# Kernel optimization log

Measured on AMD Instinct MI355X. Metric: run time of the kernel, lower is better.

## Reference

```python
import jax, jax.numpy as jnp
import numpy as np

N_GENES = 15135
N_CMT = 1000
HID = 64


def _gcn_norm(edge_index, n):
    # add self-loops, compute symmetric normalization deg^-1/2 * deg^-1/2
    loop = jnp.arange(n, dtype=edge_index.dtype)
    src = jnp.concatenate([edge_index[0], loop])
    dst = jnp.concatenate([edge_index[1], loop])
    deg = jax.ops.segment_sum(jnp.ones_like(src, dtype=jnp.float32), dst, num_segments=n)
    dinv = jnp.where(deg > 0, 1.0 / jnp.sqrt(deg), 0.0)
    return src, dst, dinv[src] * dinv[dst]


def _gcn_conv(x, W, b, src, dst, norm, n):
    h = x @ W                                  # [bs, N, H]
    m = h[:, src, :] * norm[None, :, None]     # gather messages [bs, E, H]
    out = jnp.zeros_like(h).at[:, dst, :].add(m)
    return out + b


def setup_inputs():
    key = jax.random.key(0)
    ks = jax.random.split(key, 16)
    bs, nf, hfc, ncls, E, P = 8, 64, 128, 2, 242160, 120000
    s = 0.05
    return {
        "x": jax.random.normal(ks[0], (bs, N_GENES, nf), jnp.float32),
        "batch": jnp.zeros((bs,), jnp.int32),
        "edge_index": jax.random.randint(ks[1], (2, E), 0, N_GENES),
        "path_row": jax.random.randint(ks[2], (P,), 0, N_GENES),
        "path_col": jax.random.randint(ks[3], (P,), 0, N_CMT),
        "W1": jax.random.normal(ks[4], (nf, HID), jnp.float32) * s,
        "b1": jnp.zeros((HID,), jnp.float32),
        "W2": jax.random.normal(ks[5], (HID, HID), jnp.float32) * s,
        "b2": jnp.zeros((HID,), jnp.float32),
        "W3": jax.random.normal(ks[6], (HID, HID), jnp.float32) * s,
        "b3": jnp.zeros((HID,), jnp.float32),
        "fcW": jax.random.normal(ks[7], (3 * HID, 1), jnp.float32) * s,
        "fcb": jnp.zeros((1,), jnp.float32),
        "l1W": jax.random.normal(ks[8], (N_CMT, hfc), jnp.float32) * s,
        "l1b": jnp.zeros((hfc,), jnp.float32),
        "l2W": jax.random.normal(ks[9], (hfc, ncls), jnp.float32) * s,
        "l2b": jnp.zeros((ncls,), jnp.float32),
    }


def reference(x, batch, edge_index, path_row, path_col,
              W1, b1, W2, b2, W3, b3, fcW, fcb, l1W, l1b, l2W, l2b):
    bs, n = x.shape[0], x.shape[1]
    src, dst, norm = _gcn_norm(edge_index, n)

    x1 = jax.nn.relu(_gcn_conv(x, W1, b1, src, dst, norm, n))
    x2 = jax.nn.relu(_gcn_conv(x1, W2, b2, src, dst, norm, n))
    x3 = jax.nn.relu(_gcn_conv(x2, W3, b3, src, dst, norm, n))
    # mode='cat': torch.stack(xs, -1).view(bs, N, -1) -> layout [..., h*L + l]
    xc = jnp.stack([x1, x2, x3], axis=-1).reshape(bs, n, HID * 3)

    # pathway pooling: scatter_mean(x[row], col) over node axis
    xt = jnp.transpose(xc, (1, 0, 2))            # [N, bs, F]
    g = xt[path_row]                             # [P, bs, F]
    sums = jax.ops.segment_sum(g, path_col, num_segments=N_CMT)
    cnt = jax.ops.segment_sum(jnp.ones_like(path_col, dtype=xc.dtype), path_col, num_segments=N_CMT)
    pooled = sums / jnp.maximum(cnt, 1.0)[:, None, None]   # [n_cmt, bs, F]
    pooled = jnp.transpose(pooled, (1, 0, 2)).reshape(-1, HID * 3)  # [bs*n_cmt, F]

    h = (pooled @ fcW + fcb).reshape(bs, N_CMT)   # fc -> view(-1, n_cmt)
    h = jax.nn.relu(h @ l1W + l1b)                # (dropout is identity in eval)
    h = h @ l2W + l2b
    return jax.nn.log_softmax(h, axis=-1)
```

## Files before the change

### kernel.cpp

```cpp
#include <hip/hip_runtime.h>
#include <hip/hip_bf16.h>
#include <hip/hip_fp16.h>
#include <math.h>

#define HID 64

#if defined(__has_builtin)
#if __has_builtin(__builtin_amdgcn_cvt_pk_f32_fp8) && __has_builtin(__builtin_amdgcn_cvt_pk_fp8_f32)
#define HWFP8 1
#endif
#endif

typedef float vfloat2 __attribute__((ext_vector_type(2)));


__device__ __forceinline__ unsigned short f2bf(float x) {
    unsigned int u = __float_as_uint(x);
    unsigned int r = u + 0x7fffu + ((u >> 16) & 1u);
    return (unsigned short)(r >> 16);
}

#ifndef HWFP8
__device__ __forceinline__ unsigned int enc8_sw(float a) {
    unsigned short hb = __half_as_ushort(__float2half(a));
    unsigned int r = (unsigned int)hb + 0x7fu + ((hb >> 8) & 1u);
    return (r >> 8) & 0xffu;
}
__device__ __forceinline__ float dec8_sw(unsigned int b) {
    return __half2float(__ushort_as_half((unsigned short)(b << 8)));
}
#endif

__device__ __forceinline__ unsigned int enc4(float a, float b, float c, float d) {
#ifdef HWFP8
    int r = __builtin_amdgcn_cvt_pk_fp8_f32(a, b, 0, false);
    r = __builtin_amdgcn_cvt_pk_fp8_f32(c, d, r, true);
    return (unsigned int)r;
#else
    return enc8_sw(a) | (enc8_sw(b) << 8) | (enc8_sw(c) << 16) | (enc8_sw(d) << 24);
#endif
}

__device__ __forceinline__ void dec4(unsigned int w, float* f) {
#ifdef HWFP8
    vfloat2 a = __builtin_amdgcn_cvt_pk_f32_fp8((int)w, false);
    vfloat2 b = __builtin_amdgcn_cvt_pk_f32_fp8((int)w, true);
    f[0] = a.x; f[1] = a.y; f[2] = b.x; f[3] = b.y;
#else
    f[0] = dec8_sw(w & 0xffu); f[1] = dec8_sw((w >> 8) & 0xffu);
    f[2] = dec8_sw((w >> 16) & 0xffu); f[3] = dec8_sw(w >> 24);
#endif
}

__device__ __forceinline__ void dec8(uint2 g, float* f) {
    dec4(g.x, f);
    dec4(g.y, f + 4);
}


__global__ __launch_bounds__(256) void k_pre_count(const int* __restrict__ edst, int* __restrict__ deg, int E,
                                                   const int* __restrict__ pcol, int* __restrict__ ccnt, int P) {
    int gth = blockIdx.x * blockDim.x + threadIdx.x;
    int GT = gridDim.x * blockDim.x;
    for (int e = gth; e < E; e += GT) atomicAdd(&deg[edst[e]], 1);
    for (int p = gth; p < P; p += GT) atomicAdd(&ccnt[pcol[p]], 1);
}

__global__ __launch_bounds__(256) void k_pre_scan(const int* __restrict__ deg, int* __restrict__ rowoff, int N,
                                                  const int* __restrict__ ccnt, int* __restrict__ coff, int NC,
                                                  float* __restrict__ dinv) {
    __shared__ int part[256];
    int t = threadIdx.x;
    int gth = blockIdx.x * blockDim.x + t;
    int GT = gridDim.x * blockDim.x;
    for (int i = gth; i < N; i += GT) dinv[i] = rsqrtf((float)(deg[i] + 1));

    const int* cnt = nullptr; int* off = nullptr; int n = 0;
    if (blockIdx.x == 0)      { cnt = deg;  off = rowoff; n = N; }
    else if (blockIdx.x == 1) { cnt = ccnt; off = coff;   n = NC; }
    else return;

    int CH = (n + 255) >> 8;
    int lo = min(t * CH, n), hi = min(lo + CH, n);
    int sum = 0;
    for (int i = lo; i < hi; ++i) sum += cnt[i];
    part[t] = sum;
    __syncthreads();
    for (int o = 1; o < 256; o <<= 1) {
        int v = (t >= o) ? part[t - o] : 0;
        __syncthreads();
        part[t] += v;
        __syncthreads();
    }
    int run = (t == 0) ? 0 : part[t - 1];
    for (int i = lo; i < hi; ++i) { off[i] = run; run += cnt[i]; }
    if (t == 255) off[n] = run;
}

__global__ __launch_bounds__(256) void k_pre_scatter(const int* __restrict__ esrc, const int* __restrict__ edst,
                                                     const float* __restrict__ dinv, const int* __restrict__ rowoff,
                                                     int* __restrict__ fill, int* __restrict__ ssrc,
                                                     float* __restrict__ snorm, int E,
                                                     const int* __restrict__ prow, const int* __restrict__ pcol,
                                                     const int* __restrict__ coff, int* __restrict__ cfill,
                                                     int* __restrict__ crow, int P) {
    int gth = blockIdx.x * blockDim.x + threadIdx.x;
    int GT = gridDim.x * blockDim.x;
    for (int e = gth; e < E; e += GT) {
        int s = esrc[e], d = edst[e];
        int pos = rowoff[d] + atomicAdd(&fill[d], 1);
        ssrc[pos]  = s;
        snorm[pos] = dinv[s] * dinv[d];
    }
    for (int p = gth; p < P; p += GT) {
        int c = pcol[p];
        int pos = coff[c] + atomicAdd(&cfill[c], 1);
        crow[pos] = prow[p];
    }
}


template<int MODE>
__global__ __launch_bounds__(256) void k_gemm_rt(const void* __restrict__ Xv,
                                                 const float* __restrict__ W,
                                                 unsigned int* __restrict__ Yq,
                                                 float S, int N, int rowsTot) {
    __shared__ float sW[64 * 64];
    __shared__ float sXT[64 * 68];
    int t = threadIdx.x;
    int r0 = blockIdx.x * 64;

#pragma unroll
    for (int i = 0; i < 16; ++i) sW[t + i * 256] = W[t + i * 256];

    {
        int row = t & 63;
        int kg = t >> 6;
        int gr = r0 + row;
        bool ok = gr < rowsTot;
        const float* Xf = (const float*)Xv;
        const unsigned short* Xh = (const unsigned short*)Xv;
#pragma unroll
        for (int i = 0; i < 4; ++i) {
            int k = (kg + i * 4) * 4;
            float4 v = make_float4(0.f, 0.f, 0.f, 0.f);
            if (ok) {
                if (MODE == 0) {
                    int n = gr >> 3, b = gr & 7;
                    v = *(const float4*)&Xf[((size_t)b * N + n) * 64 + k];
                } else {
                    ushort4 u = *(const ushort4*)&Xh[(size_t)gr * 64 + k];
                    v.x = __uint_as_float(((unsigned int)u.x) << 16);
                    v.y = __uint_as_float(((unsigned int)u.y) << 16);
                    v.z = __uint_as_float(((unsigned int)u.z) << 16);
                    v.w = __uint_as_float(((unsigned int)u.w) << 16);
                }
            }
            sXT[(k + 0) * 68 + row] = v.x;
            sXT[(k + 1) * 68 + row] = v.y;
            sXT[(k + 2) * 68 + row] = v.z;
            sXT[(k + 3) * 68 + row] = v.w;
        }
    }
    __syncthreads();

    int ci = t & 15, ri = t >> 4;
    float acc[4][4] = {};
#pragma unroll 16
    for (int k = 0; k < 64; ++k) {
        float4 xr = *(const float4*)&sXT[k * 68 + ri * 4];
        float4 wc = *(const float4*)&sW[k * 64 + ci * 4];
        acc[0][0] = fmaf(xr.x, wc.x, acc[0][0]); acc[0][1] = fmaf(xr.x, wc.y, acc[0][1]);
        acc[0][2] = fmaf(xr.x, wc.z, acc[0][2]); acc[0][3] = fmaf(xr.x, wc.w, acc[0][3]);
        acc[1][0] = fmaf(xr.y, wc.x, acc[1][0]); acc[1][1] = fmaf(xr.y, wc.y, acc[1][1]);
        acc[1][2] = fmaf(xr.y, wc.z, acc[1][2]); acc[1][3] = fmaf(xr.y, wc.w, acc[1][3]);
        acc[2][0] = fmaf(xr.z, wc.x, acc[2][0]); acc[2][1] = fmaf(xr.z, wc.y, acc[2][1]);
        acc[2][2] = fmaf(xr.z, wc.z, acc[2][2]); acc[2][3] = fmaf(xr.z, wc.w, acc[2][3]);
        acc[3][0] = fmaf(xr.w, wc.x, acc[3][0]); acc[3][1] = fmaf(xr.w, wc.y, acc[3][1]);
        acc[3][2] = fmaf(xr.w, wc.z, acc[3][2]); acc[3][3] = fmaf(xr.w, wc.w, acc[3][3]);
    }

#pragma unroll
    for (int j = 0; j < 4; ++j) {
        int row = r0 + ri * 4 + j;
        if (row < rowsTot)
            Yq[(size_t)row * 16 + ci] =
                enc4(acc[j][0] * S, acc[j][1] * S, acc[j][2] * S, acc[j][3] * S);
    }
}

template<int LAYER, bool STORE>
__global__ __launch_bounds__(256) void k_agg(const uint2* __restrict__ Y,
                                             const int* __restrict__ rowoff,
                                             const int* __restrict__ ssrc,
                                             const float* __restrict__ snorm,
                                             const float* __restrict__ dinv,
                                             const float* __restrict__ bias,
                                             const float* __restrict__ fcW,
                                             uint4* __restrict__ O,
                                             float* __restrict__ sArr,
                                             float invS, int N) {
    int n = blockIdx.x * 4 + (threadIdx.x >> 6);
    if (n >= N) return;
    int lane = threadIdx.x & 63;
    int hb = (lane & 7) * 8;
    float bv[8], wv[8];
#pragma unroll
    for (int k = 0; k < 8; ++k) { bv[k] = bias[hb + k]; wv[k] = fcW[3 * (hb + k) + LAYER]; }

    float dn = dinv[n];
    float w0 = dn * dn;
    float acc[8], f[8];
    dec8(Y[(size_t)n * 64 + lane], f);
#pragma unroll
    for (int k = 0; k < 8; ++k) acc[k] = w0 * f[k];

    int beg = rowoff[n], end = rowoff[n + 1];
    int i = beg;
    for (; i + 7 < end; i += 8) {
        int   sI[8];
        float wI[8];
        uint2 g[8];
#pragma unroll
        for (int u = 0; u < 8; ++u) { sI[u] = ssrc[i + u]; wI[u] = snorm[i + u]; }
#pragma unroll
        for (int u = 0; u < 8; ++u) g[u] = Y[(size_t)sI[u] * 64 + lane];
#pragma unroll
        for (int u = 0; u < 8; ++u) {
            dec8(g[u], f);
#pragma unroll
            for (int k = 0; k < 8; ++k) acc[k] = fmaf(wI[u], f[k], acc[k]);
        }
    }
    for (; i < end; ++i) {
        int s = ssrc[i];
        float w = snorm[i];
        dec8(Y[(size_t)s * 64 + lane], f);
#pragma unroll
        for (int k = 0; k < 8; ++k) acc[k] = fmaf(w, f[k], acc[k]);
    }

    float sv = 0.f;
#pragma unroll
    for (int k = 0; k < 8; ++k) {
        float o = fmaxf(fmaf(acc[k], invS, bv[k]), 0.f);
        acc[k] = o;
        sv = fmaf(o, wv[k], sv);
    }
    if (STORE) {
        uint4 o;
        o.x = (unsigned int)f2bf(acc[0]) | ((unsigned int)f2bf(acc[1]) << 16);
        o.y = (unsigned int)f2bf(acc[2]) | ((unsigned int)f2bf(acc[3]) << 16);
        o.z = (unsigned int)f2bf(acc[4]) | ((unsigned int)f2bf(acc[5]) << 16);
        o.w = (unsigned int)f2bf(acc[6]) | ((unsigned int)f2bf(acc[7]) << 16);
        O[(size_t)n * 64 + lane] = o;
    }
    sv += __shfl_down(sv, 4, 64);
    sv += __shfl_down(sv, 2, 64);
    sv += __shfl_down(sv, 1, 64);
    if ((lane & 7) == 0) {
        int b = lane >> 3;
        float* sp = sArr + (size_t)n * 8 + b;
        if (LAYER == 0) *sp = sv;
        else            *sp += sv;
    }
}


__global__ __launch_bounds__(64) void k_poolg(const float* __restrict__ sArr,
                                              const int* __restrict__ coff,
                                              const int* __restrict__ crow,
                                              float* __restrict__ hpoolT) {
    int c = blockIdx.x;
    int lane = threadIdx.x;
    int beg = coff[c], end = coff[c + 1];
    int b = lane & 7;
    float acc = 0.f;
    for (int i = beg + (lane >> 3); i < end; i += 8) {
        int r = crow[i];
        acc += sArr[(size_t)r * 8 + b];
    }
    acc += __shfl_down(acc, 32, 64);
    acc += __shfl_down(acc, 16, 64);
    acc += __shfl_down(acc, 8, 64);
    if (lane < 8) {
        float inv = 1.f / fmaxf((float)(end - beg), 1.f);
        hpoolT[(size_t)c * 8 + b] = acc * inv;
    }
}

__global__ __launch_bounds__(128) void k_l1p(const float* __restrict__ hpoolT,
                                             const float* __restrict__ fcb,
                                             const float* __restrict__ l1W,
                                             float* __restrict__ hpre,
                                             int NC, int HFC, int CHUNK) {
    __shared__ float hl[64];
    int b = blockIdx.y;
    int c0 = blockIdx.x * CHUNK;
    int j = threadIdx.x;
    int cend = min(c0 + CHUNK, NC);
    for (int c = c0 + j; c < cend; c += blockDim.x)
        hl[c - c0] = hpoolT[(size_t)c * 8 + b] + fcb[0];
    __syncthreads();
    float acc = 0.f;
    for (int c = c0; c < cend; ++c) acc = fmaf(hl[c - c0], l1W[(size_t)c * HFC + j], acc);
    atomicAdd(&hpre[(size_t)b * HFC + j], acc);
}

__global__ __launch_bounds__(256) void k_final(const float* __restrict__ hpre,
                                               const float* __restrict__ l1b,
                                               const float* __restrict__ l2W,
                                               const float* __restrict__ l2b,
                                               float* __restrict__ out,
                                               int bs, int HFC, int NCLS) {
    __shared__ float z[64];
    int t = threadIdx.x;
    int g = t >> 4, l16 = t & 15;
    int nout = bs * NCLS;
    float v = 0.f;
    int b = g / NCLS, k = g - b * NCLS;
    if (g < nout) {
        for (int j = l16; j < HFC; j += 16) {
            float h = fmaxf(hpre[(size_t)b * HFC + j] + l1b[j], 0.f);
            v = fmaf(h, l2W[(size_t)j * NCLS + k], v);
        }
    }
    v += __shfl_down(v, 8, 64);
    v += __shfl_down(v, 4, 64);
    v += __shfl_down(v, 2, 64);
    v += __shfl_down(v, 1, 64);
    if (l16 == 0 && g < nout) z[g] = v + l2b[k];
    __syncthreads();
    if (t < bs) {
        float m = -1e30f;
        for (int c = 0; c < NCLS; ++c) m = fmaxf(m, z[t * NCLS + c]);
        float s = 0.f;
        for (int c = 0; c < NCLS; ++c) s += expf(z[t * NCLS + c] - m);
        float lse = m + logf(s);
        for (int c = 0; c < NCLS; ++c) out[t * NCLS + c] = z[t * NCLS + c] - lse;
    }
}


extern "C" void kernel_launch(void* const* d_in, const int* in_sizes, int n_in,
                              void* d_out, int out_size, void* d_ws, size_t ws_size,
                              hipStream_t stream) {
    const float* x   = (const float*)d_in[0];
    const int* eidx  = (const int*)d_in[2];
    const int* prow  = (const int*)d_in[3];
    const int* pcol  = (const int*)d_in[4];
    const float* W1  = (const float*)d_in[5];
    const float* b1  = (const float*)d_in[6];
    const float* W2  = (const float*)d_in[7];
    const float* b2  = (const float*)d_in[8];
    const float* W3  = (const float*)d_in[9];
    const float* b3  = (const float*)d_in[10];
    const float* fcW = (const float*)d_in[11];
    const float* fcb = (const float*)d_in[12];
    const float* l1W = (const float*)d_in[13];
    const float* l1b = (const float*)d_in[14];
    const float* l2W = (const float*)d_in[15];
    const float* l2b = (const float*)d_in[16];
    float* out = (float*)d_out;

    const int bs   = in_sizes[1];
    const int E    = in_sizes[2] / 2;
    const int P    = in_sizes[3];
    const int N    = in_sizes[0] / (bs * HID);
    const int HFC  = in_sizes[14];
    const int NC   = in_sizes[13] / HFC;
    const int NCLS = in_sizes[15] / HFC;
    const int rows = N * bs;

    const int* esrc = eidx;
    const int* edst = eidx + E;

    size_t off = 0;
    auto alloc = [&](size_t bytes) -> void* {
        void* r = (char*)d_ws + off;
        off += (bytes + 255) & ~(size_t)255;
        return r;
    };
    char* zbase   = (char*)d_ws;
    int*   deg    = (int*)  alloc((size_t)N * 4);
    int*   fill   = (int*)  alloc((size_t)N * 4);
    int*   ccnt   = (int*)  alloc((size_t)NC * 4);
    int*   cfill  = (int*)  alloc((size_t)NC * 4);
    float* hpre   = (float*)alloc((size_t)bs * HFC * 4);
    size_t zspan  = off;
    float* dinv   = (float*)alloc((size_t)N * 4);
    int*   rowoff = (int*)  alloc(((size_t)N + 1) * 4);
    int*   coff   = (int*)  alloc(((size_t)NC + 1) * 4);
    int*   crow   = (int*)  alloc((size_t)P * 4);
    float* hpoolT = (float*)alloc((size_t)NC * bs * 4);
    int*   ssrc   = (int*)  alloc((size_t)E * 4);
    float* snorm  = (float*)alloc((size_t)E * 4);
    unsigned int* Yq   = (unsigned int*)alloc((size_t)rows * HID);
    unsigned short* X1 = (unsigned short*)alloc((size_t)rows * HID * 2);
    unsigned short* X2 = (unsigned short*)alloc((size_t)rows * HID * 2);
    float* sArr   = (float*)alloc((size_t)rows * 4);

    hipMemsetAsync(zbase, 0, zspan, stream);

    int gPre = 512;
    k_pre_count<<<gPre, 256, 0, stream>>>(edst, deg, E, pcol, ccnt, P);
    k_pre_scan<<<64, 256, 0, stream>>>(deg, rowoff, N, ccnt, coff, NC, dinv);
    k_pre_scatter<<<gPre, 256, 0, stream>>>(esrc, edst, dinv, rowoff, fill, ssrc, snorm, E,
                                            prow, pcol, coff, cfill, crow, P);

    const float S1 = 1.f,  iS1 = 1.f;
    const float S2 = 16.f, iS2 = 1.f / 16.f;
    const float S3 = 128.f, iS3 = 1.f / 128.f;

    int gG = (rows + 63) / 64;
    int gA = (N + 3) / 4;
    k_gemm_rt<0><<<gG, 256, 0, stream>>>(x, W1, Yq, S1, N, rows);
    k_agg<0, true><<<gA, 256, 0, stream>>>((const uint2*)Yq, rowoff, ssrc, snorm, dinv, b1, fcW, (uint4*)X1, sArr, iS1, N);
    k_gemm_rt<1><<<gG, 256, 0, stream>>>(X1, W2, Yq, S2, N, rows);
    k_agg<1, true><<<gA, 256, 0, stream>>>((const uint2*)Yq, rowoff, ssrc, snorm, dinv, b2, fcW, (uint4*)X2, sArr, iS2, N);
    k_gemm_rt<1><<<gG, 256, 0, stream>>>(X2, W3, Yq, S3, N, rows);
    k_agg<2, false><<<gA, 256, 0, stream>>>((const uint2*)Yq, rowoff, ssrc, snorm, dinv, b3, fcW, nullptr, sArr, iS3, N);

    k_poolg<<<NC, 64, 0, stream>>>(sArr, coff, crow, hpoolT);

    const int CHUNK = 40;
    dim3 gL1((NC + CHUNK - 1) / CHUNK, bs);
    k_l1p<<<gL1, 128, 0, stream>>>(hpoolT, fcb, l1W, hpre, NC, HFC, CHUNK);
    k_final<<<1, 256, 0, stream>>>(hpre, l1b, l2W, l2b, out, bs, HFC, NCLS);
}
```

Measured before the change: 377.3 us.

## Fuse pooling, linear head and softmax into one last-block kernel

Merges the three tail kernels (pathway pooling, l1 partial GEMM with atomics, final l2 + log-softmax) into a single launch. Each wave pools one pathway with a 4-way unrolled gather, and the last block to finish, found through an atomic counter with threadfences, runs the full l1 matvec serially over all pathways and then the l2 + log-softmax. This removes two kernel launches and the hpre atomics. In exchange, the l1 matvec over 1000 pathways now runs in a single block instead of being spread across many.

```diff
diff --git a/kernel.cpp b/kernel.cpp
--- a/kernel.cpp
+++ b/kernel.cpp
@@ -266,78 +266,95 @@
     }
 }
 
-
-__global__ __launch_bounds__(64) void k_poolg(const float* __restrict__ sArr,
+__global__ __launch_bounds__(256) void k_head(const float* __restrict__ sArr,
                                               const int* __restrict__ coff,
                                               const int* __restrict__ crow,
-                                              float* __restrict__ hpoolT) {
-    int c = blockIdx.x;
-    int lane = threadIdx.x;
-    int beg = coff[c], end = coff[c + 1];
-    int b = lane & 7;
-    float acc = 0.f;
-    for (int i = beg + (lane >> 3); i < end; i += 8) {
-        int r = crow[i];
-        acc += sArr[(size_t)r * 8 + b];
-    }
-    acc += __shfl_down(acc, 32, 64);
-    acc += __shfl_down(acc, 16, 64);
-    acc += __shfl_down(acc, 8, 64);
-    if (lane < 8) {
-        float inv = 1.f / fmaxf((float)(end - beg), 1.f);
-        hpoolT[(size_t)c * 8 + b] = acc * inv;
-    }
-}
-
-__global__ __launch_bounds__(128) void k_l1p(const float* __restrict__ hpoolT,
-                                             const float* __restrict__ fcb,
-                                             const float* __restrict__ l1W,
-                                             float* __restrict__ hpre,
-                                             int NC, int HFC, int CHUNK) {
-    __shared__ float hl[64];
-    int b = blockIdx.y;
-    int c0 = blockIdx.x * CHUNK;
-    int j = threadIdx.x;
-    int cend = min(c0 + CHUNK, NC);
-    for (int c = c0 + j; c < cend; c += blockDim.x)
-        hl[c - c0] = hpoolT[(size_t)c * 8 + b] + fcb[0];
-    __syncthreads();
-    float acc = 0.f;
-    for (int c = c0; c < cend; ++c) acc = fmaf(hl[c - c0], l1W[(size_t)c * HFC + j], acc);
-    atomicAdd(&hpre[(size_t)b * HFC + j], acc);
-}
-
-__global__ __launch_bounds__(256) void k_final(const float* __restrict__ hpre,
-                                               const float* __restrict__ l1b,
-                                               const float* __restrict__ l2W,
-                                               const float* __restrict__ l2b,
-                                               float* __restrict__ out,
-                                               int bs, int HFC, int NCLS) {
-    __shared__ float z[64];
+                                              float* __restrict__ hpoolT,
+                                              int* __restrict__ done,
+                                              const float* __restrict__ fcb,
+                                              const float* __restrict__ l1W,
+                                              const float* __restrict__ l1b,
+                                              const float* __restrict__ l2W,
+                                              const float* __restrict__ l2b,
+                                              float* __restrict__ out,
+                                              int NC, int HFC, int bs, int NCLS) {
     int t = threadIdx.x;
+    int lane = t & 63;
+    int wv = t >> 6;
+    float fcb0 = fcb[0];
+
+    for (int c = blockIdx.x * 4 + wv; c < NC; c += gridDim.x * 4) {
+        int beg = coff[c], end = coff[c + 1];
+        int b = lane & 7;
+        float acc = 0.f;
+        int i = beg + (lane >> 3);
+        for (; i + 24 < end; i += 32) {
+            int r0 = crow[i], r1 = crow[i + 8], r2 = crow[i + 16], r3 = crow[i + 24];
+            float a0 = sArr[(size_t)r0 * 8 + b];
+            float a1 = sArr[(size_t)r1 * 8 + b];
+            float a2 = sArr[(size_t)r2 * 8 + b];
+            float a3 = sArr[(size_t)r3 * 8 + b];
+            acc += (a0 + a1) + (a2 + a3);
+        }
+        for (; i < end; i += 8) acc += sArr[(size_t)crow[i] * 8 + b];
+        acc += __shfl_down(acc, 32, 64);
+        acc += __shfl_down(acc, 16, 64);
+        acc += __shfl_down(acc, 8, 64);
+        if (lane < 8) {
+            float inv = 1.f / fmaxf((float)(end - beg), 1.f);
+            hpoolT[(size_t)c * 8 + b] = acc * inv + fcb0;
+        }
+    }
+
+    __threadfence();
+    __syncthreads();
+    __shared__ int amLast;
+    if (t == 0) amLast = (atomicAdd(done, 1) == gridDim.x - 1);
+    __syncthreads();
+    if (!amLast) return;
+    __threadfence();
+
+    __shared__ float sH[8 * 128];
+    int j = t & 127;
+    int bb = t >> 7;
+    float ac0 = 0.f, ac1 = 0.f, ac2 = 0.f, ac3 = 0.f;
+    for (int c = 0; c < NC; ++c) {
+        float w = l1W[(size_t)c * HFC + j];
+        const float* hp = &hpoolT[(size_t)c * 8];
+        ac0 = fmaf(hp[bb + 0], w, ac0);
+        ac1 = fmaf(hp[bb + 2], w, ac1);
+        ac2 = fmaf(hp[bb + 4], w, ac2);
+        ac3 = fmaf(hp[bb + 6], w, ac3);
+    }
+    float lb = l1b[j];
+    sH[(bb + 0) * 128 + j] = fmaxf(ac0 + lb, 0.f);
+    sH[(bb + 2) * 128 + j] = fmaxf(ac1 + lb, 0.f);
+    sH[(bb + 4) * 128 + j] = fmaxf(ac2 + lb, 0.f);
+    sH[(bb + 6) * 128 + j] = fmaxf(ac3 + lb, 0.f);
+    __syncthreads();
+
+    __shared__ float sZ[64];
     int g = t >> 4, l16 = t & 15;
     int nout = bs * NCLS;
     float v = 0.f;
-    int b = g / NCLS, k = g - b * NCLS;
+    int b2 = g / NCLS, k2 = g - b2 * NCLS;
     if (g < nout) {
-        for (int j = l16; j < HFC; j += 16) {
-            float h = fmaxf(hpre[(size_t)b * HFC + j] + l1b[j], 0.f);
-            v = fmaf(h, l2W[(size_t)j * NCLS + k], v);
-        }
+        for (int jj = l16; jj < HFC; jj += 16)
+            v = fmaf(sH[b2 * 128 + jj], l2W[(size_t)jj * NCLS + k2], v);
     }
     v += __shfl_down(v, 8, 64);
     v += __shfl_down(v, 4, 64);
     v += __shfl_down(v, 2, 64);
     v += __shfl_down(v, 1, 64);
-    if (l16 == 0 && g < nout) z[g] = v + l2b[k];
+    if (l16 == 0 && g < nout) sZ[g] = v + l2b[k2];
     __syncthreads();
     if (t < bs) {
         float m = -1e30f;
-        for (int c = 0; c < NCLS; ++c) m = fmaxf(m, z[t * NCLS + c]);
+        for (int c = 0; c < NCLS; ++c) m = fmaxf(m, sZ[t * NCLS + c]);
         float s = 0.f;
-        for (int c = 0; c < NCLS; ++c) s += expf(z[t * NCLS + c] - m);
+        for (int c = 0; c < NCLS; ++c) s += expf(sZ[t * NCLS + c] - m);
         float lse = m + logf(s);
-        for (int c = 0; c < NCLS; ++c) out[t * NCLS + c] = z[t * NCLS + c] - lse;
+        for (int c = 0; c < NCLS; ++c) out[t * NCLS + c] = sZ[t * NCLS + c] - lse;
     }
 }
 
@@ -386,7 +403,7 @@
     int*   fill   = (int*)  alloc((size_t)N * 4);
     int*   ccnt   = (int*)  alloc((size_t)NC * 4);
     int*   cfill  = (int*)  alloc((size_t)NC * 4);
-    float* hpre   = (float*)alloc((size_t)bs * HFC * 4);
+    int*   done   = (int*)  alloc(4);
     size_t zspan  = off;
     float* dinv   = (float*)alloc((size_t)N * 4);
     int*   rowoff = (int*)  alloc(((size_t)N + 1) * 4);
@@ -421,10 +438,7 @@
     k_gemm_rt<1><<<gG, 256, 0, stream>>>(X2, W3, Yq, S3, N, rows);
     k_agg<2, false><<<gA, 256, 0, stream>>>((const uint2*)Yq, rowoff, ssrc, snorm, dinv, b3, fcW, nullptr, sArr, iS3, N);
 
-    k_poolg<<<NC, 64, 0, stream>>>(sArr, coff, crow, hpoolT);
-
-    const int CHUNK = 40;
-    dim3 gL1((NC + CHUNK - 1) / CHUNK, bs);
-    k_l1p<<<gL1, 128, 0, stream>>>(hpoolT, fcb, l1W, hpre, NC, HFC, CHUNK);
-    k_final<<<1, 256, 0, stream>>>(hpre, l1b, l2W, l2b, out, bs, HFC, NCLS);
-}
+    int gH = (NC + 3) / 4;
+    k_head<<<gH, 256, 0, stream>>>(sArr, coff, crow, hpoolT, done, fcb, l1W, l1b, l2W, l2b, out,
+                                   NC, HFC, bs, NCLS);
+}
```

After: 617.0 us. 1.64x slower.
